# Performance work log

Measured on AMD Instinct MI355X. Metric: run time of the kernel, lower is better.

## Reference

```python
import jax, jax.numpy as jnp
import numpy as np

N_E = 4096
E_DIM = 256
BETA = 0.25


def setup_inputs() -> dict:
    key = jax.random.key(0)
    k1, k2 = jax.random.split(key)
    z = jax.random.normal(k1, (2, E_DIM, 8, 32, 32), dtype=jnp.float32)
    # torch: embedding.weight.data.uniform_(-1/n_e, 1/n_e)
    embedding_weight = jax.random.uniform(
        k2, (N_E, E_DIM), dtype=jnp.float32, minval=-1.0 / N_E, maxval=1.0 / N_E)
    ema_embedding = jnp.zeros((N_E, E_DIM), dtype=jnp.float32)
    return {"z": z, "embedding_weight": embedding_weight, "ema_embedding": ema_embedding}


def reference(z, embedding_weight, ema_embedding):
    sg = jax.lax.stop_gradient
    # [B, C, D, H, W] -> [B, D, H, W, C]
    zp = jnp.transpose(z, (0, 2, 3, 4, 1))
    zf = zp.reshape(-1, E_DIM)  # [N, e_dim]
    # pairwise squared distances: ||z||^2 + ||e||^2 - 2 z e^T  -> [N, n_e]
    d = (jnp.sum(zf * zf, axis=1, keepdims=True)
         + jnp.sum(embedding_weight * embedding_weight, axis=1)
         - 2.0 * jnp.matmul(zf, embedding_weight.T))
    min_encoding_indices = jnp.argmin(d, axis=1)  # [N]
    min_encodings = jax.nn.one_hot(min_encoding_indices, N_E, dtype=zf.dtype)  # [N, n_e]
    # one_hot @ W == gather of codebook rows
    z_q = embedding_weight[min_encoding_indices].reshape(zp.shape)
    loss = (jnp.mean((sg(z_q) - zp) ** 2)
            + BETA * jnp.mean((z_q - sg(zp)) ** 2))
    # straight-through estimator
    z_q_st = zp + sg(z_q - zp)
    # EMA buffer update (torch does this under no_grad)
    ema_new = BETA * ema_embedding + (1.0 - BETA) * sg(embedding_weight)
    e_mean = jnp.mean(min_encodings, axis=0)
    perplexity = jnp.exp(-jnp.sum(e_mean * jnp.log(e_mean + 1e-10)))
    z_q_out = jnp.transpose(z_q_st, (0, 4, 1, 2, 3))
    z_out = jnp.transpose(zp, (0, 4, 1, 2, 3))
    return (loss, z_q_out, perplexity, min_encodings,
            min_encoding_indices[:, None], z_out, ema_new)
```

## Files before the change

kernel.cpp:

```cpp
#include <hip/hip_runtime.h>
#include <math.h>


#define N_E    4096
#define EDIM   256
#define SPAT   8192
#define NROWS  16384
#define ZELEMS 4194304
#define NCHUNK 32
#define NLOSSPARTS 16384

#define OFF_LOSS    0
#define OFF_ZQ      1
#define OFF_PERP    4194305
#define OFF_ONEHOT  4194306
#define OFF_IDX     71303170
#define OFF_ZOUT    71319554
#define OFF_EMA     75513858

#define SCR_WH_F   4
#define SCR_WL_F   524292
#define SCR_BI_F   71319556
#define SCR_BDD_F  71843844
#define SCR_ZH_F   72892420

#define MARG 1.5e-4f
#define GAPM 1.5e-4f

typedef unsigned short u16;
typedef short short8 __attribute__((ext_vector_type(8)));
typedef float f32x4 __attribute__((ext_vector_type(4)));
typedef const void __attribute__((address_space(1)))* gas1;
typedef void __attribute__((address_space(3)))* las3;
#define GLOAD16(g, l) __builtin_amdgcn_global_load_lds((gas1)(g), (las3)(l), 16, 0, 0)

__device__ __forceinline__ u16 f2bf(float f) {
    unsigned u = __float_as_uint(f);
    return (u16)((u + 0x7fffu + ((u >> 16) & 1u)) >> 16);
}
__device__ __forceinline__ float bf2f(u16 h) {
    return __uint_as_float(((unsigned)h) << 16);
}

__global__ __launch_bounds__(256) void prep_w_kernel(
        const float* __restrict__ W, const float* __restrict__ ema,
        u16* __restrict__ wh, u16* __restrict__ wl,
        float* __restrict__ se, float* __restrict__ out_ema) {
    const size_t t = (size_t)blockIdx.x * 256 + threadIdx.x;
    const int code = (int)(t >> 6);
    const int lane = threadIdx.x & 63;

    const float4 v = *(const float4*)(W + t * 4);

    u16 h0 = f2bf(v.x), h1 = f2bf(v.y), h2 = f2bf(v.z), h3 = f2bf(v.w);
    u16 l0 = f2bf(v.x - bf2f(h0)), l1 = f2bf(v.y - bf2f(h1));
    u16 l2 = f2bf(v.z - bf2f(h2)), l3 = f2bf(v.w - bf2f(h3));
    uint2 hp, lp;
    hp.x = (unsigned)h0 | ((unsigned)h1 << 16); hp.y = (unsigned)h2 | ((unsigned)h3 << 16);
    lp.x = (unsigned)l0 | ((unsigned)l1 << 16); lp.y = (unsigned)l2 | ((unsigned)l3 << 16);
    *(uint2*)(wh + t * 4) = hp;
    *(uint2*)(wl + t * 4) = lp;

    const float4 e4 = *(const float4*)(ema + t * 4);
    float4 o4;
    o4.x = 0.25f * e4.x + 0.75f * v.x;
    o4.y = 0.25f * e4.y + 0.75f * v.y;
    o4.z = 0.25f * e4.z + 0.75f * v.z;
    o4.w = 0.25f * e4.w + 0.75f * v.w;
    *(float4*)(out_ema + t * 4) = o4;

    float s = v.x * v.x + v.y * v.y + v.z * v.z + v.w * v.w;
    #pragma unroll
    for (int off = 32; off > 0; off >>= 1) s += __shfl_down(s, off);
    if (lane == 0) se[code] = s;
}

__global__ __launch_bounds__(512) void rnorm_kernel(const float* __restrict__ z,
                                                    float* __restrict__ sz) {
    const int r0 = blockIdx.x * 128;
    const int bb = r0 >> 13;
    const int sp0 = r0 & (SPAT - 1);
    const float* zb = z + (size_t)bb * (EDIM * SPAT) + sp0;
    __shared__ float szp[4][128];
    const int lr = threadIdx.x & 127, kq = threadIdx.x >> 7;
    float s = 0.f;
    const float* p = zb + lr + (size_t)(kq * 64) * SPAT;
    for (int k = 0; k < 64; ++k) {
        float v = p[(size_t)k * SPAT];
        s += v * v;
    }
    szp[kq][lr] = s;
    __syncthreads();
    if (threadIdx.x < 128)
        sz[r0 + threadIdx.x] =
            ((szp[0][threadIdx.x] + szp[1][threadIdx.x]) + szp[2][threadIdx.x]) + szp[3][threadIdx.x];
}

__global__ __launch_bounds__(256) void split_z_kernel(const float* __restrict__ z,
                                                      u16* __restrict__ zh) {
    __shared__ float t[128][65];
    const int tid = threadIdx.x, wid = tid >> 6, lane = tid & 63;
    const int sp0 = blockIdx.x * 64, c0 = blockIdx.y * 128, b = blockIdx.z;
    const float* zb = z + (size_t)b * (EDIM * SPAT);
    #pragma unroll
    for (int it = 0; it < 32; ++it) {
        const int cl = wid + 4 * it;
        t[cl][lane] = zb[(size_t)(c0 + cl) * SPAT + sp0 + lane];
    }
    __syncthreads();
    #pragma unroll
    for (int it = 0; it < 16; ++it) {
        const int r = wid + 4 * it;
        const float v0 = t[2 * lane][r], v1 = t[2 * lane + 1][r];
        const u16 h0 = f2bf(v0), h1 = f2bf(v1);
        const size_t row = (size_t)b * SPAT + sp0 + r;
        ((unsigned*)zh)[row * 128 + (c0 >> 1) + lane] = (unsigned)h0 | ((unsigned)h1 << 16);
    }
}

__global__ __launch_bounds__(256, 3) void argmin_kernel(
        const u16* __restrict__ zh,
        const u16* __restrict__ wh, const u16* __restrict__ wl,
        const float* __restrict__ se, const float* __restrict__ sz,
        float* __restrict__ bDD, int* __restrict__ bI,
        float* __restrict__ out_onehot) {
    __shared__ u16 sW[2][128][64];
    __shared__ u16 sZ[2][128][32];
    __shared__ float mD[2][128];
    __shared__ int   mI[2][128];
    __shared__ float mD2[2][128];

    const int tid = threadIdx.x;
    const int wid = tid >> 6, lane = tid & 63;
    const int wm = wid >> 1, wn = wid & 1;
    const int lq = lane >> 4, lr = lane & 15;
    const int chunk = blockIdx.y;
    const int rbase = blockIdx.x * 128;
    const int cbase = chunk * 128;

    const u16* gw[4];
    #pragma unroll
    for (int i = 0; i < 4; ++i) {
        const int o = i * 256 + tid;
        const int row = o >> 3, g = o & 7, u = g ^ (row & 7);
        const int ks = (u & 3) * 8;
        gw[i] = (u < 4 ? wh : wl) + (size_t)(cbase + row) * EDIM + ks;
    }
    const u16* gz[2];
    #pragma unroll
    for (int j = 0; j < 2; ++j) {
        const int o = j * 256 + tid;
        const int row = o >> 2, g = o & 3, u = g ^ ((row >> 1) & 3);
        gz[j] = zh + (size_t)(rbase + row) * EDIM + u * 8;
    }

    char* sWb = (char*)&sW[0][0][0];
    char* sZb = (char*)&sZ[0][0][0];

    int aoff[4][2], boff[4];
    #pragma unroll
    for (int tt = 0; tt < 4; ++tt) {
        const int cl = wn * 64 + tt * 16 + lr;
        const int s0 = lq ^ (cl & 7);
        aoff[tt][0] = cl * 128 + s0 * 16;
        aoff[tt][1] = cl * 128 + (s0 ^ 4) * 16;
        const int rl = wm * 64 + tt * 16 + lr;
        boff[tt] = rl * 64 + (lq ^ ((rl >> 1) & 3)) * 16;
    }

    f32x4 acc[4][4];
    #pragma unroll
    for (int ci = 0; ci < 4; ++ci)
        #pragma unroll
        for (int rj = 0; rj < 4; ++rj) {
            f32x4 zzz = {0.f, 0.f, 0.f, 0.f};
            acc[ci][rj] = zzz;
        }

    #define STAGE(b) do {                                                      \
        _Pragma("unroll")                                                      \
        for (int i = 0; i < 4; ++i) {                                          \
            GLOAD16(gw[i], sWb + (b) * 16384 + (i * 256 + wid * 64) * 16);     \
            gw[i] += 32;                                                       \
        }                                                                      \
        _Pragma("unroll")                                                      \
        for (int j = 0; j < 2; ++j) {                                          \
            GLOAD16(gz[j], sZb + (b) * 8192 + (j * 256 + wid * 64) * 16);      \
            gz[j] += 32;                                                       \
        }                                                                      \
    } while (0)

    STAGE(0);
    __syncthreads();

    for (int k0 = 0; k0 < 8; ++k0) {
        const int cur = k0 & 1;
        if (k0 < 7) STAGE(cur ^ 1);

        const char* wbase = sWb + cur * 16384;
        const char* zbase = sZb + cur * 8192;
        short8 zb[4];
        #pragma unroll
        for (int rj = 0; rj < 4; ++rj)
            zb[rj] = *(const short8*)(zbase + boff[rj]);
        #pragma unroll
        for (int ci = 0; ci < 4; ++ci) {
            const short8 wah = *(const short8*)(wbase + aoff[ci][0]);
            const short8 wal = *(const short8*)(wbase + aoff[ci][1]);
            #pragma unroll
            for (int rj = 0; rj < 4; ++rj) {
                acc[ci][rj] = __builtin_amdgcn_mfma_f32_16x16x32_bf16(wah, zb[rj], acc[ci][rj], 0, 0, 0);
                acc[ci][rj] = __builtin_amdgcn_mfma_f32_16x16x32_bf16(wal, zb[rj], acc[ci][rj], 0, 0, 0);
            }
        }
        __syncthreads();
    }
    #undef STAGE

    f32x4 sev[4];
    #pragma unroll
    for (int ci = 0; ci < 4; ++ci)
        sev[ci] = *(const f32x4*)(se + cbase + wn * 64 + ci * 16 + lq * 4);

    #pragma unroll
    for (int rj = 0; rj < 4; ++rj) {
        const int rloc = wm * 64 + rj * 16 + lr;
        const float szr = sz[rbase + rloc];
        float b1 = 3.4e38f, b2 = 3.4e38f; int bi1 = 0x7fffffff;
        #pragma unroll
        for (int ci = 0; ci < 4; ++ci) {
            #pragma unroll
            for (int r = 0; r < 4; ++r) {
                const float q = (szr + sev[ci][r]) - 2.0f * acc[ci][rj][r];
                const int code = cbase + wn * 64 + ci * 16 + lq * 4 + r;
                if (q < b1 || (q == b1 && code < bi1)) {
                    b2 = b1; b1 = q; bi1 = code;
                } else if (q < b2) {
                    b2 = q;
                }
            }
        }
        #pragma unroll
        for (int mask = 16; mask <= 32; mask <<= 1) {
            const float od1 = __shfl_xor(b1, mask);
            const int   oi1 = __shfl_xor(bi1, mask);
            const float od2 = __shfl_xor(b2, mask);
            const bool ot = (od1 < b1) || (od1 == b1 && oi1 < bi1);
            if (ot) { b2 = fminf(b1, od2); b1 = od1; bi1 = oi1; }
            else    { b2 = fminf(b2, od1); }
        }
        if (lq == 0) {
            mD[wn][rloc]  = b1;
            mI[wn][rloc]  = bi1;
            mD2[wn][rloc] = b2;
        }
    }
    __syncthreads();
    if (tid < 128) {
        const float d0 = mD[0][tid], d1 = mD[1][tid];
        const int   i0 = mI[0][tid], i1 = mI[1][tid];
        const float s0 = mD2[0][tid], s1 = mD2[1][tid];
        float dm, sm; int im;
        if (d1 < d0 || (d1 == d0 && i1 < i0)) { dm = d1; im = i1; sm = fminf(s1, d0); }
        else                                  { dm = d0; im = i0; sm = fminf(s0, d1); }
        const int row = rbase + tid;
        float2 p; p.x = dm; p.y = sm;
        *(float2*)(bDD + (size_t)row * 64 + chunk * 2) = p;
        bI[(size_t)row * 32 + chunk] = im;
    }

    {
        const int slice = blockIdx.x * 32 + blockIdx.y;
        float* oh = out_onehot + (size_t)slice * 16384;
        const float4 z4 = {0.f, 0.f, 0.f, 0.f};
        #pragma unroll
        for (int it = 0; it < 16; ++it)
            *(float4*)(oh + it * 1024 + tid * 4) = z4;
    }
}

__global__ __launch_bounds__(256) void resolve_kernel(
        const float* __restrict__ z, const float* __restrict__ W,
        const float* __restrict__ se, const float* __restrict__ sz,
        const float* __restrict__ bDD, const int* __restrict__ bI,
        int* __restrict__ idx_ws, float* __restrict__ out_idx,
        float* __restrict__ out_onehot) {
    __shared__ float zr[EDIM];
    __shared__ float rd[128];
    __shared__ int   ri[128];
    __shared__ unsigned smask;
    __shared__ int swin, sskip;
    const int row = blockIdx.x;
    const int tid = threadIdx.x;

    if (tid < 64) {
        const int c = tid & 31;
        const float2 dd = *(const float2*)(bDD + (size_t)row * 64 + c * 2);
        const int    i1 = bI[(size_t)row * 32 + c];
        const float d1 = dd.x;
        float b1 = dd.x, b2 = dd.y; int j1 = i1;
        #pragma unroll
        for (int mask = 16; mask > 0; mask >>= 1) {
            const float od1 = __shfl_xor(b1, mask);
            const int   oj1 = __shfl_xor(j1, mask);
            const float od2 = __shfl_xor(b2, mask);
            const bool ot = (od1 < b1) || (od1 == b1 && oj1 < j1);
            if (ot) { b2 = fminf(b1, od2); b1 = od1; j1 = oj1; }
            else    { b2 = fminf(b2, od1); }
        }
        const unsigned long long m = __ballot(d1 <= b1 + MARG);
        if (tid == 0) {
            smask = (unsigned)(m & 0xffffffffu);
            swin  = j1;
            sskip = (b2 - b1 > GAPM) ? 1 : 0;
        }
    }
    __syncthreads();

    if (sskip) {
        if (tid == 0) {
            idx_ws[row]  = swin;
            out_idx[row] = (float)swin;
            out_onehot[(size_t)row * N_E + swin] = 1.0f;
        }
        return;
    }

    {
        const int b = row >> 13, sp = row & (SPAT - 1);
        zr[tid] = z[(size_t)b * (EDIM * SPAT) + (size_t)tid * SPAT + sp];
    }
    __syncthreads();

    const float szr = sz[row];
    unsigned cmask = smask;
    float best = 3.4e38f; int bi = 0x7fffffff;
    while (cmask) {
        const int cc = __ffs(cmask) - 1;
        cmask &= cmask - 1;
        if (tid < 128) {
            const int code = cc * 128 + tid;
            const float* wr = W + (size_t)code * EDIM;
            float s = 0.f;
            for (int k = 0; k < EDIM; ++k) s += zr[k] * wr[k];
            const float q = (szr + se[code]) - 2.0f * s;
            if (q < best || (q == best && code < bi)) { best = q; bi = code; }
        }
    }
    if (tid < 128) { rd[tid] = best; ri[tid] = bi; }
    __syncthreads();
    for (int off = 64; off > 0; off >>= 1) {
        if (tid < off) {
            const float od = rd[tid + off]; const int oi = ri[tid + off];
            if (od < rd[tid] || (od == rd[tid] && oi < ri[tid])) {
                rd[tid] = od; ri[tid] = oi;
            }
        }
        __syncthreads();
    }
    if (tid == 0) {
        const int ii = ri[0];
        idx_ws[row]  = ii;
        out_idx[row] = (float)ii;
        out_onehot[(size_t)row * N_E + ii] = 1.0f;
    }
}

__global__ __launch_bounds__(256) void outputs_kernel(
        const float* __restrict__ z, const float* __restrict__ W,
        const int* __restrict__ idx,
        float* __restrict__ zq_out, float* __restrict__ z_out,
        double* __restrict__ loss_parts) {
    const int t  = blockIdx.x * 256 + threadIdx.x;
    const float zv = z[t];
    const int sp = t & (SPAT - 1);
    const int c  = (t >> 13) & 255;
    const int b  = t >> 21;
    const int n  = (b << 13) + sp;
    const int id = idx[n];
    const float e    = W[id * EDIM + c];
    const float diff = e - zv;
    zq_out[t] = zv + diff;
    z_out[t]  = zv;

    double ds = (double)(diff * diff);
    #pragma unroll
    for (int off = 32; off > 0; off >>= 1) ds += __shfl_down(ds, off);
    __shared__ double bsum[4];
    const int lane = threadIdx.x & 63, w = threadIdx.x >> 6;
    if (lane == 0) bsum[w] = ds;
    __syncthreads();
    if (threadIdx.x == 0)
        loss_parts[blockIdx.x] = bsum[0] + bsum[1] + bsum[2] + bsum[3];
}

__global__ __launch_bounds__(1024) void final_kernel(
        const int* __restrict__ idx, const double* __restrict__ loss_parts,
        float* __restrict__ out_loss, float* __restrict__ out_perp) {
    __shared__ int   hist[N_E];
    __shared__ float ps[1024];
    __shared__ double ls[1024];
    const int tid = threadIdx.x;

    for (int i = tid; i < N_E; i += 1024) hist[i] = 0;
    __syncthreads();
    for (int r = tid; r < NROWS; r += 1024) atomicAdd(&hist[idx[r]], 1);
    __syncthreads();

    float s = 0.f;
    for (int c = tid; c < N_E; c += 1024) {
        const float p = (float)hist[c] * (1.0f / (float)NROWS);
        s += p * logf(p + 1e-10f);
    }
    double l = 0.0;
    for (int c = tid; c < NLOSSPARTS; c += 1024) l += loss_parts[c];
    ps[tid] = s;
    ls[tid] = l;
    __syncthreads();
    for (int off = 512; off > 0; off >>= 1) {
        if (tid < off) {
            ps[tid] += ps[tid + off];
            ls[tid] += ls[tid + off];
        }
        __syncthreads();
    }
    if (tid == 0) {
        *out_perp = expf(-ps[0]);
        const float m = (float)(ls[0] / (double)ZELEMS);
        *out_loss = m + 0.25f * m;
    }
}

extern "C" void kernel_launch(void* const* d_in, const int* in_sizes, int n_in,
                              void* d_out, int out_size, void* d_ws, size_t ws_size,
                              hipStream_t stream) {
    const float* z   = (const float*)d_in[0];
    const float* W   = (const float*)d_in[1];
    const float* ema = (const float*)d_in[2];
    float* out = (float*)d_out;

    float* out_loss   = out + OFF_LOSS;
    float* out_zq     = out + OFF_ZQ;
    float* out_perp   = out + OFF_PERP;
    float* out_onehot = out + OFF_ONEHOT;
    float* out_idx    = out + OFF_IDX;
    float* out_z      = out + OFF_ZOUT;
    float* out_ema    = out + OFF_EMA;

    u16*   wh  = (u16*)(out + SCR_WH_F);
    u16*   wl  = (u16*)(out + SCR_WL_F);
    int*   bI  = (int*)(out + SCR_BI_F);
    float* bDD = out + SCR_BDD_F;
    u16*   zh  = (u16*)(out + SCR_ZH_F);

    char* ws = (char*)d_ws;
    float*  se    = (float*)ws;
    float*  sz    = (float*)(ws + 16384);
    int*    idxb  = (int*)  (ws + 81920);
    double* lossp = (double*)(ws + 147456);

    prep_w_kernel<<<1024, 256, 0, stream>>>(W, ema, wh, wl, se, out_ema);
    rnorm_kernel<<<128, 512, 0, stream>>>(z, sz);
    split_z_kernel<<<dim3(128, 2, 2), 256, 0, stream>>>(z, zh);
    argmin_kernel<<<dim3(NROWS / 128, NCHUNK), 256, 0, stream>>>(
        zh, wh, wl, se, sz, bDD, bI, out_onehot);
    resolve_kernel<<<NROWS, 256, 0, stream>>>(z, W, se, sz, bDD, bI,
                                              idxb, out_idx, out_onehot);
    outputs_kernel<<<ZELEMS / 256, 256, 0, stream>>>(z, W, idxb, out_zq, out_z,
                                                     lossp);
    final_kernel<<<1, 1024, 0, stream>>>(idxb, lossp, out_loss, out_perp);
}
```

Before: 551.8 us.

## Merge prep kernels into one launch, shrink resolve blocks, parallelize histogram

Fuses the codebook prep, z row-norm and z bf16 split kernels into a single launch partitioned by block index, and has that launch also zero a global histogram. The resolve kernel now runs with 128 threads instead of 256, so no half-idle threads sit in the candidate loop. The codebook usage histogram moves out of the single-block final kernel into a 16-block kernel with shared-memory atomics followed by global atomics. This cuts launch count and serial single-block work, at the cost of one extra small launch and global atomics.

```diff
diff --git a/kernel.cpp b/kernel.cpp
--- a/kernel.cpp
+++ b/kernel.cpp
@@ -27,6 +27,12 @@
 #define MARG 1.5e-4f
 #define GAPM 1.5e-4f
 
+#define PB_W0   0
+#define PB_Z0   1024
+#define PB_N0   1536
+#define PB_H0   1664
+#define PB_TOT  1668
+
 typedef unsigned short u16;
 typedef short short8 __attribute__((ext_vector_type(8)));
 typedef float f32x4 __attribute__((ext_vector_type(4)));
@@ -42,79 +48,88 @@
     return __uint_as_float(((unsigned)h) << 16);
 }
 
-__global__ __launch_bounds__(256) void prep_w_kernel(
+__global__ __launch_bounds__(256) void prep_all_kernel(
         const float* __restrict__ W, const float* __restrict__ ema,
+        const float* __restrict__ z,
         u16* __restrict__ wh, u16* __restrict__ wl,
-        float* __restrict__ se, float* __restrict__ out_ema) {
-    const size_t t = (size_t)blockIdx.x * 256 + threadIdx.x;
-    const int code = (int)(t >> 6);
-    const int lane = threadIdx.x & 63;
-
-    const float4 v = *(const float4*)(W + t * 4);
-
-    u16 h0 = f2bf(v.x), h1 = f2bf(v.y), h2 = f2bf(v.z), h3 = f2bf(v.w);
-    u16 l0 = f2bf(v.x - bf2f(h0)), l1 = f2bf(v.y - bf2f(h1));
-    u16 l2 = f2bf(v.z - bf2f(h2)), l3 = f2bf(v.w - bf2f(h3));
-    uint2 hp, lp;
-    hp.x = (unsigned)h0 | ((unsigned)h1 << 16); hp.y = (unsigned)h2 | ((unsigned)h3 << 16);
-    lp.x = (unsigned)l0 | ((unsigned)l1 << 16); lp.y = (unsigned)l2 | ((unsigned)l3 << 16);
-    *(uint2*)(wh + t * 4) = hp;
-    *(uint2*)(wl + t * 4) = lp;
-
-    const float4 e4 = *(const float4*)(ema + t * 4);
-    float4 o4;
-    o4.x = 0.25f * e4.x + 0.75f * v.x;
-    o4.y = 0.25f * e4.y + 0.75f * v.y;
-    o4.z = 0.25f * e4.z + 0.75f * v.z;
-    o4.w = 0.25f * e4.w + 0.75f * v.w;
-    *(float4*)(out_ema + t * 4) = o4;
-
-    float s = v.x * v.x + v.y * v.y + v.z * v.z + v.w * v.w;
-    #pragma unroll
-    for (int off = 32; off > 0; off >>= 1) s += __shfl_down(s, off);
-    if (lane == 0) se[code] = s;
-}
-
-__global__ __launch_bounds__(512) void rnorm_kernel(const float* __restrict__ z,
-                                                    float* __restrict__ sz) {
-    const int r0 = blockIdx.x * 128;
-    const int bb = r0 >> 13;
-    const int sp0 = r0 & (SPAT - 1);
-    const float* zb = z + (size_t)bb * (EDIM * SPAT) + sp0;
+        float* __restrict__ se, float* __restrict__ out_ema,
+        u16* __restrict__ zh, float* __restrict__ sz,
+        int* __restrict__ ghist) {
+    __shared__ float t[128][65];
     __shared__ float szp[4][128];
-    const int lr = threadIdx.x & 127, kq = threadIdx.x >> 7;
-    float s = 0.f;
-    const float* p = zb + lr + (size_t)(kq * 64) * SPAT;
-    for (int k = 0; k < 64; ++k) {
-        float v = p[(size_t)k * SPAT];
-        s += v * v;
-    }
-    szp[kq][lr] = s;
-    __syncthreads();
-    if (threadIdx.x < 128)
-        sz[r0 + threadIdx.x] =
-            ((szp[0][threadIdx.x] + szp[1][threadIdx.x]) + szp[2][threadIdx.x]) + szp[3][threadIdx.x];
-}
-
-__global__ __launch_bounds__(256) void split_z_kernel(const float* __restrict__ z,
-                                                      u16* __restrict__ zh) {
-    __shared__ float t[128][65];
-    const int tid = threadIdx.x, wid = tid >> 6, lane = tid & 63;
-    const int sp0 = blockIdx.x * 64, c0 = blockIdx.y * 128, b = blockIdx.z;
-    const float* zb = z + (size_t)b * (EDIM * SPAT);
-    #pragma unroll
-    for (int it = 0; it < 32; ++it) {
-        const int cl = wid + 4 * it;
-        t[cl][lane] = zb[(size_t)(c0 + cl) * SPAT + sp0 + lane];
-    }
-    __syncthreads();
-    #pragma unroll
-    for (int it = 0; it < 16; ++it) {
-        const int r = wid + 4 * it;
-        const float v0 = t[2 * lane][r], v1 = t[2 * lane + 1][r];
-        const u16 h0 = f2bf(v0), h1 = f2bf(v1);
-        const size_t row = (size_t)b * SPAT + sp0 + r;
-        ((unsigned*)zh)[row * 128 + (c0 >> 1) + lane] = (unsigned)h0 | ((unsigned)h1 << 16);
+    const int bx  = blockIdx.x;
+    const int tid = threadIdx.x;
+
+    if (bx < PB_Z0) {
+        const size_t tt = (size_t)bx * 256 + tid;
+        const int code = (int)(tt >> 6);
+        const int lane = tid & 63;
+        const float4 v = *(const float4*)(W + tt * 4);
+
+        u16 h0 = f2bf(v.x), h1 = f2bf(v.y), h2 = f2bf(v.z), h3 = f2bf(v.w);
+        u16 l0 = f2bf(v.x - bf2f(h0)), l1 = f2bf(v.y - bf2f(h1));
+        u16 l2 = f2bf(v.z - bf2f(h2)), l3 = f2bf(v.w - bf2f(h3));
+        uint2 hp, lp;
+        hp.x = (unsigned)h0 | ((unsigned)h1 << 16); hp.y = (unsigned)h2 | ((unsigned)h3 << 16);
+        lp.x = (unsigned)l0 | ((unsigned)l1 << 16); lp.y = (unsigned)l2 | ((unsigned)l3 << 16);
+        *(uint2*)(wh + tt * 4) = hp;
+        *(uint2*)(wl + tt * 4) = lp;
+
+        const float4 e4 = *(const float4*)(ema + tt * 4);
+        float4 o4;
+        o4.x = 0.25f * e4.x + 0.75f * v.x;
+        o4.y = 0.25f * e4.y + 0.75f * v.y;
+        o4.z = 0.25f * e4.z + 0.75f * v.z;
+        o4.w = 0.25f * e4.w + 0.75f * v.w;
+        *(float4*)(out_ema + tt * 4) = o4;
+
+        float s = v.x * v.x + v.y * v.y + v.z * v.z + v.w * v.w;
+        #pragma unroll
+        for (int off = 32; off > 0; off >>= 1) s += __shfl_down(s, off);
+        if (lane == 0) se[code] = s;
+    } else if (bx < PB_N0) {
+        const int sub = bx - PB_Z0;
+        const int sp0 = (sub & 127) * 64, c0 = ((sub >> 7) & 1) * 128, b = sub >> 8;
+        const int wid = tid >> 6, lane = tid & 63;
+        const float* zb = z + (size_t)b * (EDIM * SPAT);
+        #pragma unroll
+        for (int it = 0; it < 32; ++it) {
+            const int cl = wid + 4 * it;
+            t[cl][lane] = zb[(size_t)(c0 + cl) * SPAT + sp0 + lane];
+        }
+        __syncthreads();
+        #pragma unroll
+        for (int it = 0; it < 16; ++it) {
+            const int r = wid + 4 * it;
+            const float v0 = t[2 * lane][r], v1 = t[2 * lane + 1][r];
+            const u16 h0 = f2bf(v0), h1 = f2bf(v1);
+            const size_t row = (size_t)b * SPAT + sp0 + r;
+            ((unsigned*)zh)[row * 128 + (c0 >> 1) + lane] = (unsigned)h0 | ((unsigned)h1 << 16);
+        }
+    } else if (bx < PB_H0) {
+        const int r0 = (bx - PB_N0) * 128;
+        const int bb = r0 >> 13;
+        const int sp0 = r0 & (SPAT - 1);
+        const float* zb = z + (size_t)bb * (EDIM * SPAT) + sp0;
+        const int lr = tid & 127, kh = tid >> 7;
+        #pragma unroll
+        for (int h = 0; h < 2; ++h) {
+            const int kq = kh * 2 + h;
+            float s = 0.f;
+            const float* p = zb + lr + (size_t)(kq * 64) * SPAT;
+            for (int k = 0; k < 64; ++k) {
+                float v = p[(size_t)k * SPAT];
+                s += v * v;
+            }
+            szp[kq][lr] = s;
+        }
+        __syncthreads();
+        if (tid < 128)
+            sz[r0 + tid] = ((szp[0][tid] + szp[1][tid]) + szp[2][tid]) + szp[3][tid];
+    } else {
+        const int base = (bx - PB_H0) * 1024;
+        #pragma unroll
+        for (int j = 0; j < 4; ++j) ghist[base + j * 256 + tid] = 0;
     }
 }
 
@@ -279,7 +294,7 @@
     }
 }
 
-__global__ __launch_bounds__(256) void resolve_kernel(
+__global__ __launch_bounds__(128) void resolve_kernel(
         const float* __restrict__ z, const float* __restrict__ W,
         const float* __restrict__ se, const float* __restrict__ sz,
         const float* __restrict__ bDD, const int* __restrict__ bI,
@@ -328,7 +343,8 @@
 
     {
         const int b = row >> 13, sp = row & (SPAT - 1);
-        zr[tid] = z[(size_t)b * (EDIM * SPAT) + (size_t)tid * SPAT + sp];
+        zr[tid]       = z[(size_t)b * (EDIM * SPAT) + (size_t)tid * SPAT + sp];
+        zr[tid + 128] = z[(size_t)b * (EDIM * SPAT) + (size_t)(tid + 128) * SPAT + sp];
     }
     __syncthreads();
 
@@ -338,16 +354,14 @@
     while (cmask) {
         const int cc = __ffs(cmask) - 1;
         cmask &= cmask - 1;
-        if (tid < 128) {
-            const int code = cc * 128 + tid;
-            const float* wr = W + (size_t)code * EDIM;
-            float s = 0.f;
-            for (int k = 0; k < EDIM; ++k) s += zr[k] * wr[k];
-            const float q = (szr + se[code]) - 2.0f * s;
-            if (q < best || (q == best && code < bi)) { best = q; bi = code; }
-        }
-    }
-    if (tid < 128) { rd[tid] = best; ri[tid] = bi; }
+        const int code = cc * 128 + tid;
+        const float* wr = W + (size_t)code * EDIM;
+        float s = 0.f;
+        for (int k = 0; k < EDIM; ++k) s += zr[k] * wr[k];
+        const float q = (szr + se[code]) - 2.0f * s;
+        if (q < best || (q == best && code < bi)) { best = q; bi = code; }
+    }
+    rd[tid] = best; ri[tid] = bi;
     __syncthreads();
     for (int off = 64; off > 0; off >>= 1) {
         if (tid < off) {
@@ -363,6 +377,20 @@
         idx_ws[row]  = ii;
         out_idx[row] = (float)ii;
         out_onehot[(size_t)row * N_E + ii] = 1.0f;
+    }
+}
+
+__global__ __launch_bounds__(1024) void hist_kernel(const int* __restrict__ idx,
+                                                    int* __restrict__ ghist) {
+    __shared__ int lh[N_E];
+    const int tid = threadIdx.x;
+    for (int i = tid; i < N_E; i += 1024) lh[i] = 0;
+    __syncthreads();
+    atomicAdd(&lh[idx[blockIdx.x * 1024 + tid]], 1);
+    __syncthreads();
+    for (int c = tid; c < N_E; c += 1024) {
+        const int v = lh[c];
+        if (v) atomicAdd(&ghist[c], v);
     }
 }
 
@@ -395,21 +423,15 @@
 }
 
 __global__ __launch_bounds__(1024) void final_kernel(
-        const int* __restrict__ idx, const double* __restrict__ loss_parts,
+        const int* __restrict__ ghist, const double* __restrict__ loss_parts,
         float* __restrict__ out_loss, float* __restrict__ out_perp) {
-    __shared__ int   hist[N_E];
     __shared__ float ps[1024];
     __shared__ double ls[1024];
     const int tid = threadIdx.x;
 
-    for (int i = tid; i < N_E; i += 1024) hist[i] = 0;
-    __syncthreads();
-    for (int r = tid; r < NROWS; r += 1024) atomicAdd(&hist[idx[r]], 1);
-    __syncthreads();
-
     float s = 0.f;
     for (int c = tid; c < N_E; c += 1024) {
-        const float p = (float)hist[c] * (1.0f / (float)NROWS);
+        const float p = (float)ghist[c] * (1.0f / (float)NROWS);
         s += p * logf(p + 1e-10f);
     }
     double l = 0.0;
@@ -458,15 +480,16 @@
     float*  sz    = (float*)(ws + 16384);
     int*    idxb  = (int*)  (ws + 81920);
     double* lossp = (double*)(ws + 147456);
-
-    prep_w_kernel<<<1024, 256, 0, stream>>>(W, ema, wh, wl, se, out_ema);
-    rnorm_kernel<<<128, 512, 0, stream>>>(z, sz);
-    split_z_kernel<<<dim3(128, 2, 2), 256, 0, stream>>>(z, zh);
+    int*    ghist = (int*)  (ws + 278528);
+
+    prep_all_kernel<<<PB_TOT, 256, 0, stream>>>(W, ema, z, wh, wl, se, out_ema,
+                                                zh, sz, ghist);
     argmin_kernel<<<dim3(NROWS / 128, NCHUNK), 256, 0, stream>>>(
         zh, wh, wl, se, sz, bDD, bI, out_onehot);
-    resolve_kernel<<<NROWS, 256, 0, stream>>>(z, W, se, sz, bDD, bI,
+    resolve_kernel<<<NROWS, 128, 0, stream>>>(z, W, se, sz, bDD, bI,
                                               idxb, out_idx, out_onehot);
+    hist_kernel<<<16, 1024, 0, stream>>>(idxb, ghist);
     outputs_kernel<<<ZELEMS / 256, 256, 0, stream>>>(z, W, idxb, out_zq, out_z,
                                                      lossp);
-    final_kernel<<<1, 1024, 0, stream>>>(idxb, lossp, out_loss, out_perp);
-}
+    final_kernel<<<1, 1024, 0, stream>>>(ghist, lossp, out_loss, out_perp);
+}
```

After: 550.5 us. Within noise of the previous version (-0.2%).
